# Kernel optimization log

Measured on AMD Instinct MI355X. Metric: run time of the kernel, lower is better.

The kernel has to match this reference:

```python
import jax, jax.numpy as jnp
import numpy as np

NUM_EMBEDDINGS = 512
EMBEDDING_DIM = 64
COMMITMENT_COST = 0.25
DECAY = 0.99
EPSILON = 1e-05


def setup_inputs() -> dict:
    key = jax.random.key(0)
    k1, k2, k3 = jax.random.split(key, 3)
    inputs = jax.random.normal(k1, (32, 64, 64, EMBEDDING_DIM), dtype=jnp.float32)
    emb_w = jax.random.normal(k2, (NUM_EMBEDDINGS, EMBEDDING_DIM), dtype=jnp.float32)
    ema_cluster_size = jnp.ones((NUM_EMBEDDINGS,), dtype=jnp.float32)
    ema_w = jax.random.normal(k3, (NUM_EMBEDDINGS, EMBEDDING_DIM), dtype=jnp.float32)
    return {"inputs": inputs, "emb_w": emb_w,
            "ema_cluster_size": ema_cluster_size, "ema_w": ema_w}


def reference(inputs, emb_w, ema_cluster_size, ema_w):
    """VQ-VAE EMA quantizer forward (training=True path).

    inputs:           [B, H, W, D]  NHWC latents
    emb_w:            [K, D]        codebook (pre-update)
    ema_cluster_size: [K]           EMA cluster-size buffer
    ema_w:            [K, D]        EMA weight buffer
    """
    B, H, W, D = inputs.shape
    K = emb_w.shape[0]
    flat = inputs.reshape(-1, D)                                  # [N, D]

    distances = (jnp.sum(flat * flat, axis=1, keepdims=True)
                 - 2.0 * flat @ emb_w.T
                 + jnp.sum(emb_w * emb_w, axis=1))
    encoding_indices = jnp.argmin(distances, axis=1)              # [N]
    encodings = jax.nn.one_hot(encoding_indices, K, dtype=flat.dtype)  # [N, K]

    # --- EMA codebook update (buffer math; no gradient flows here) ---
    counts = jax.lax.stop_gradient(jnp.sum(encodings, axis=0))    # [K]
    cs = ema_cluster_size * DECAY + (1.0 - DECAY) * counts
    n = jnp.sum(cs)
    cs = (cs + EPSILON) / (n + K * EPSILON) * n                   # Laplace smoothing
    dw = jax.ops.segment_sum(jax.lax.stop_gradient(flat),
                             encoding_indices, num_segments=K)    # [K, D]
    new_ema_w = ema_w * DECAY + (1.0 - DECAY) * dw
    new_emb = new_ema_w / cs[:, None]                             # updated codebook

    # Quantize with the updated codebook (gather)
    quantized = new_emb[encoding_indices].reshape(B, H, W, D)

    # Commitment loss (quantized is detached)
    e_latent_loss = jnp.mean((jax.lax.stop_gradient(quantized) - inputs) ** 2)
    loss = COMMITMENT_COST * e_latent_loss

    # Straight-through estimator
    quantized_st = inputs + jax.lax.stop_gradient(quantized - inputs)

    avg_probs = jnp.mean(encodings, axis=0)
    perplexity = jnp.exp(-jnp.sum(avg_probs * jnp.log(avg_probs + 1e-10)))

    # NHWC -> NCHW as in the original return
    return loss, jnp.transpose(quantized_st, (0, 3, 1, 2)), perplexity, encodings
```

## Files before the change

kernel.cpp:

```cpp
#include <hip/hip_runtime.h>

#define DIM 64
#define K_CODES 512
#define N_VEC 131072
#define NREP 16
#define Q_OFF 1
#define PERP_OFF 8388609
#define ENC_OFF 8388610

using bfrag = __attribute__((ext_vector_type(8))) short;
using ffrag = __attribute__((ext_vector_type(4))) float;

__device__ __forceinline__ void split3(float x, short& h0, short& h1, short& h2)
{
    unsigned u0 = __float_as_uint(x);
    h0 = (short)(u0 >> 16);
    float r = x - __uint_as_float(u0 & 0xFFFF0000u);
    unsigned u1 = __float_as_uint(r);
    h1 = (short)(u1 >> 16);
    float r2 = r - __uint_as_float(u1 & 0xFFFF0000u);
    h2 = (short)(__float_as_uint(r2) >> 16);
}

__global__ __launch_bounds__(256) void enc_zero_kernel(float* __restrict__ enc)
{
    const size_t nf4 = 16777215;
    float4* body = reinterpret_cast<float4*>(enc + 2);
    const size_t stride = (size_t)gridDim.x * 256;
    const float4 z = make_float4(0.f, 0.f, 0.f, 0.f);
    for (size_t i = (size_t)blockIdx.x * 256 + threadIdx.x; i < nf4; i += stride)
        body[i] = z;
    if (blockIdx.x == 0 && threadIdx.x == 0) {
        enc[0] = 0.f; enc[1] = 0.f;
        enc[67108862] = 0.f; enc[67108863] = 0.f;
    }
}

__global__ __launch_bounds__(64) void ee_kernel(const float* __restrict__ emb_w,
                                                float* __restrict__ ee)
{
    const int k = blockIdx.x * 64 + threadIdx.x;
    const float4* e4 = reinterpret_cast<const float4*>(emb_w + (size_t)k * DIM);
    float s0 = 0, s1 = 0, s2 = 0, s3 = 0;
#pragma unroll
    for (int d4 = 0; d4 < 16; ++d4) {
        const float4 v = e4[d4];
        s0 = fmaf(v.x, v.x, s0); s1 = fmaf(v.y, v.y, s1);
        s2 = fmaf(v.z, v.z, s2); s3 = fmaf(v.w, v.w, s3);
    }
    ee[k] = (s0 + s1) + (s2 + s3);
}

__global__ __launch_bounds__(256) void epack_kernel(const float* __restrict__ emb_w,
                                                    bfrag* __restrict__ epack)
{
    const int t = blockIdx.x * 256 + threadIdx.x;
    const int lane = t & 63;
    const int db = (t >> 6) & 1;
    const int ct = t >> 7;
    const int c  = ct * 16 + (lane & 15);
    const int d0 = db * 32 + (lane >> 4) * 8;
    const float* src = emb_w + (size_t)c * DIM + d0;
    bfrag f0, f1, f2;
#pragma unroll
    for (int j = 0; j < 8; ++j) {
        short a, b, cc;
        split3(src[j], a, b, cc);
        f0[j] = a; f1[j] = b; f2[j] = cc;
    }
    const int base = (ct * 2 + db) * 3;
    epack[(base + 0) * 64 + lane] = f0;
    epack[(base + 1) * 64 + lane] = f1;
    epack[(base + 2) * 64 + lane] = f2;
}

__global__ __launch_bounds__(256, 1) void argmin_mfma_kernel(
    const float* __restrict__ inputs,
    const bfrag* __restrict__ epack,
    const float* __restrict__ eeg,
    int* __restrict__ idx,
    float* __restrict__ counts_rep,
    float* __restrict__ enc)
{
    const int t = threadIdx.x;
    const int w = t >> 6;
    const int lane = t & 63;
    const int r16 = lane & 15;
    const int quad = lane >> 4;
    const size_t v0 = (size_t)blockIdx.x * 128 + w * 32;

    bfrag xf[2][2][3];
#pragma unroll
    for (int rt = 0; rt < 2; ++rt)
#pragma unroll
        for (int db = 0; db < 2; ++db) {
            const float* src = inputs + (v0 + rt * 16 + r16) * DIM + db * 32 + quad * 8;
            const float4 va = *reinterpret_cast<const float4*>(src);
            const float4 vb = *reinterpret_cast<const float4*>(src + 4);
            float vals[8] = {va.x, va.y, va.z, va.w, vb.x, vb.y, vb.z, vb.w};
            bfrag f0, f1, f2;
#pragma unroll
            for (int j = 0; j < 8; ++j) {
                short a, b, c;
                split3(vals[j], a, b, c);
                f0[j] = a; f1[j] = b; f2[j] = c;
            }
            xf[rt][db][0] = f0; xf[rt][db][1] = f1; xf[rt][db][2] = f2;
        }

    float best[2][4];
    int bestk[2][4];
#pragma unroll
    for (int a = 0; a < 2; ++a)
#pragma unroll
        for (int b = 0; b < 4; ++b) { best[a][b] = 3.4e38f; bestk[a][b] = 0; }

    constexpr int PI[6] = {0, 0, 1, 0, 2, 1};
    constexpr int PJ[6] = {0, 1, 0, 2, 0, 1};

    bfrag eC[2][3];
    float eelC;
#pragma unroll
    for (int db = 0; db < 2; ++db)
#pragma unroll
        for (int s = 0; s < 3; ++s)
            eC[db][s] = epack[(db * 3 + s) * 64 + lane];
    eelC = eeg[r16];

    for (int ct = 0; ct < 32; ++ct) {
        bfrag eN[2][3];
        float eelN = 0.f;
        if (ct < 31) {
#pragma unroll
            for (int db = 0; db < 2; ++db)
#pragma unroll
                for (int s = 0; s < 3; ++s)
                    eN[db][s] = epack[(((ct + 1) * 2 + db) * 3 + s) * 64 + lane];
            eelN = eeg[(ct + 1) * 16 + r16];
        }

        ffrag acc[2];
        acc[0] = (ffrag){0.f, 0.f, 0.f, 0.f};
        acc[1] = (ffrag){0.f, 0.f, 0.f, 0.f};
#pragma unroll
        for (int db = 0; db < 2; ++db)
#pragma unroll
            for (int p = 0; p < 6; ++p) {
                acc[0] = __builtin_amdgcn_mfma_f32_16x16x32_bf16(
                    xf[0][db][PI[p]], eC[db][PJ[p]], acc[0], 0, 0, 0);
                acc[1] = __builtin_amdgcn_mfma_f32_16x16x32_bf16(
                    xf[1][db][PI[p]], eC[db][PJ[p]], acc[1], 0, 0, 0);
            }

        const int kc = ct * 16 + r16;
#pragma unroll
        for (int rt = 0; rt < 2; ++rt)
#pragma unroll
            for (int rg = 0; rg < 4; ++rg) {
                const float dist = fmaf(-2.f, acc[rt][rg], eelC);
                if (dist < best[rt][rg]) { best[rt][rg] = dist; bestk[rt][rg] = kc; }
            }

#pragma unroll
        for (int db = 0; db < 2; ++db)
#pragma unroll
            for (int s = 0; s < 3; ++s)
                eC[db][s] = eN[db][s];
        eelC = eelN;
    }

#pragma unroll
    for (int rt = 0; rt < 2; ++rt)
#pragma unroll
        for (int rg = 0; rg < 4; ++rg) {
            float b = best[rt][rg];
            int k = bestk[rt][rg];
#pragma unroll
            for (int m = 1; m < 16; m <<= 1) {
                const float ob = __shfl_xor(b, m, 64);
                const int ok = __shfl_xor(k, m, 64);
                if (ob < b || (ob == b && ok < k)) { b = ob; k = ok; }
            }
            bestk[rt][rg] = k;
        }

    if (r16 == 0) {
        float* crep = counts_rep + (blockIdx.x & (NREP - 1)) * K_CODES;
#pragma unroll
        for (int rt = 0; rt < 2; ++rt)
#pragma unroll
            for (int rg = 0; rg < 4; ++rg) {
                const int v = rt * 16 + quad * 4 + rg;
                const int k = bestk[rt][rg];
                idx[v0 + v] = k;
                atomicAdd(&crep[k], 1.0f);
                enc[(v0 + v) * (size_t)K_CODES + k] = 1.0f;
            }
    }
}

__global__ __launch_bounds__(256) void dw_scatter_kernel(
    const float* __restrict__ inputs,
    const int* __restrict__ idx,
    float* __restrict__ dwrep)
{
    __shared__ int sIdx[256];
    const int t = threadIdx.x;
    const size_t vbase = (size_t)blockIdx.x * 256;
    sIdx[t] = idx[vbase + t];
    __syncthreads();
    const int w = t >> 6, lane = t & 63;
    const int v0 = w * 64;
#pragma unroll 4
    for (int j = 0; j < 64; ++j) {
        const int v = v0 + j;
        const int k = sIdx[v];
        const float xv = inputs[(vbase + v) * DIM + lane];
        atomicAdd(&dwrep[((v & (NREP - 1)) << 15) + (k << 6) + lane], xv);
    }
}

__global__ __launch_bounds__(512) void emaA_kernel(
    const float* __restrict__ counts_rep,
    const float* __restrict__ ema_cs,
    float* __restrict__ csbuf,
    float* __restrict__ perp_out)
{
    __shared__ float red[K_CODES];
    const int k = threadIdx.x;
    float cnt = 0.f;
#pragma unroll
    for (int r = 0; r < NREP; ++r) cnt += counts_rep[r * K_CODES + k];
    float cs = ema_cs[k] * 0.99f + 0.01f * cnt;

    red[k] = cs;
    __syncthreads();
    for (int s = K_CODES / 2; s > 0; s >>= 1) {
        if (k < s) red[k] += red[k + s];
        __syncthreads();
    }
    const float n = red[0];
    __syncthreads();

    csbuf[k] = (cs + 1e-5f) / (n + (float)K_CODES * 1e-5f) * n;

    const float p = cnt * (1.0f / (float)N_VEC);
    red[k] = p * logf(p + 1e-10f);
    __syncthreads();
    for (int s = K_CODES / 2; s > 0; s >>= 1) {
        if (k < s) red[k] += red[k + s];
        __syncthreads();
    }
    if (k == 0) perp_out[0] = expf(-red[0]);
}

__global__ __launch_bounds__(256) void emaB_kernel(
    const float* __restrict__ dwrep,
    const float* __restrict__ ema_w,
    const float* __restrict__ csbuf,
    float* __restrict__ new_emb)
{
    const int t = blockIdx.x * 256 + threadIdx.x;
    const int k = t >> 6;
    float dwv = 0.f;
#pragma unroll
    for (int r = 0; r < NREP; ++r) dwv += dwrep[(r << 15) + t];
    const float v = ema_w[t] * 0.99f + 0.01f * dwv;
    new_emb[t] = v / csbuf[k];
}

__global__ __launch_bounds__(256) void quantize_kernel(
    const float* __restrict__ inputs,
    const int* __restrict__ idx,
    const float* __restrict__ new_emb,
    float* __restrict__ out_q,
    float* __restrict__ loss_accum)
{
    __shared__ int sIdx[64];
    __shared__ float tile[DIM][65];
    __shared__ float wsum[4];

    const int bh = blockIdx.x;
    const int b = bh >> 6, h = bh & 63;
    const int t = threadIdx.x;

    if (t < 64) sIdx[t] = idx[bh * 64 + t];
    __syncthreads();

    const float* inRow = inputs + (size_t)bh * 64 * DIM;
    const int d = t & 63;
    const int wg = t >> 6;
    float lsum = 0.f;
#pragma unroll
    for (int p = 0; p < 16; ++p) {
        const int w = wg * 16 + p;
        const float xv = inRow[w * DIM + d];
        const float qv = new_emb[sIdx[w] * DIM + d];
        const float diff = qv - xv;
        tile[d][w] = xv + diff;
        lsum = fmaf(diff, diff, lsum);
    }
    __syncthreads();

    const int w2 = t & 63;
    const int dg = t >> 6;
#pragma unroll
    for (int p = 0; p < 16; ++p) {
        const int d2 = dg * 16 + p;
        out_q[(((size_t)b * DIM + d2) * 64 + h) * 64 + w2] = tile[d2][w2];
    }

    for (int off = 32; off > 0; off >>= 1) lsum += __shfl_down(lsum, off);
    if ((t & 63) == 0) wsum[t >> 6] = lsum;
    __syncthreads();
    if (t == 0) atomicAdd(loss_accum, (wsum[0] + wsum[1]) + (wsum[2] + wsum[3]));
}

__global__ void finalize_kernel(const float* __restrict__ loss_accum,
                                float* __restrict__ out_loss)
{
    out_loss[0] = 0.25f * (loss_accum[0] / 8388608.0f);
}

extern "C" void kernel_launch(void* const* d_in, const int* in_sizes, int n_in,
                              void* d_out, int out_size, void* d_ws, size_t ws_size,
                              hipStream_t stream)
{
    const float* inputs = (const float*)d_in[0];
    const float* emb_w  = (const float*)d_in[1];
    const float* ema_cs = (const float*)d_in[2];
    const float* ema_w  = (const float*)d_in[3];
    float* out = (float*)d_out;
    float* ws  = (float*)d_ws;

    int*   idxbuf  = (int*)ws;
    float* crep    = ws + 131072;
    float* lossac  = ws + 139264;
    float* csbuf   = ws + 139265;
    float* eebuf   = ws + 139777;
    float* nemb    = ws + 140289;
    bfrag* epack   = (bfrag*)(ws + 173060);

    float* dwrep = out + 16;

    hipMemsetAsync(crep, 0, (NREP * K_CODES + 1) * sizeof(float), stream);
    hipMemsetAsync(dwrep, 0, NREP * K_CODES * DIM * sizeof(float), stream);

    ee_kernel<<<K_CODES / 64, 64, 0, stream>>>(emb_w, eebuf);
    epack_kernel<<<16, 256, 0, stream>>>(emb_w, epack);

    enc_zero_kernel<<<2048, 256, 0, stream>>>(out + ENC_OFF);

    argmin_mfma_kernel<<<N_VEC / 128, 256, 0, stream>>>(
        inputs, epack, eebuf, idxbuf, crep, out + ENC_OFF);

    dw_scatter_kernel<<<N_VEC / 256, 256, 0, stream>>>(inputs, idxbuf, dwrep);

    emaA_kernel<<<1, K_CODES, 0, stream>>>(crep, ema_cs, csbuf, out + PERP_OFF);
    emaB_kernel<<<K_CODES * DIM / 256, 256, 0, stream>>>(dwrep, ema_w, csbuf, nemb);

    quantize_kernel<<<32 * 64, 256, 0, stream>>>(
        inputs, idxbuf, nemb, out + Q_OFF, lossac);

    finalize_kernel<<<1, 1, 0, stream>>>(lossac, out);
}
```

Before: 226.0 us.

## Fuse one-hot write and dw scatter into argmin kernel, halve rows per wave

Drops the separate zero-fill kernel for the encodings matrix. The argmin kernel now writes each full one-hot row with float2 stores. The dw segment-sum scatter is also folded into the argmin kernel, rebuilding x from its three bf16 splits already held in registers instead of re-reading inputs. Each wave now handles 16 rows instead of 32, with two blocks per CU. This removes a 256MB zero pass and a kernel launch, but halves MFMA reuse of each codebook fragment and relies on the bf16 split sum reproducing x exactly.

```diff
diff --git a/kernel.cpp b/kernel.cpp
--- a/kernel.cpp
+++ b/kernel.cpp
@@ -22,24 +22,15 @@
     h2 = (short)(__float_as_uint(r2) >> 16);
 }
 
-__global__ __launch_bounds__(256) void enc_zero_kernel(float* __restrict__ enc)
-{
-    const size_t nf4 = 16777215;
-    float4* body = reinterpret_cast<float4*>(enc + 2);
-    const size_t stride = (size_t)gridDim.x * 256;
-    const float4 z = make_float4(0.f, 0.f, 0.f, 0.f);
-    for (size_t i = (size_t)blockIdx.x * 256 + threadIdx.x; i < nf4; i += stride)
-        body[i] = z;
-    if (blockIdx.x == 0 && threadIdx.x == 0) {
-        enc[0] = 0.f; enc[1] = 0.f;
-        enc[67108862] = 0.f; enc[67108863] = 0.f;
-    }
-}
-
-__global__ __launch_bounds__(64) void ee_kernel(const float* __restrict__ emb_w,
-                                                float* __restrict__ ee)
-{
-    const int k = blockIdx.x * 64 + threadIdx.x;
+__device__ __forceinline__ float b2f(short h)
+{
+    return __uint_as_float(((unsigned)(unsigned short)h) << 16);
+}
+
+__global__ __launch_bounds__(512) void ee_kernel(const float* __restrict__ emb_w,
+                                                 float* __restrict__ ee)
+{
+    const int k = threadIdx.x;
     const float4* e4 = reinterpret_cast<const float4*>(emb_w + (size_t)k * DIM);
     float s0 = 0, s1 = 0, s2 = 0, s3 = 0;
 #pragma unroll
@@ -74,46 +65,44 @@
     epack[(base + 2) * 64 + lane] = f2;
 }
 
-__global__ __launch_bounds__(256, 1) void argmin_mfma_kernel(
+__global__ __launch_bounds__(256, 2) void argmin_mfma_kernel(
     const float* __restrict__ inputs,
     const bfrag* __restrict__ epack,
     const float* __restrict__ eeg,
     int* __restrict__ idx,
     float* __restrict__ counts_rep,
+    float* __restrict__ dwrep,
     float* __restrict__ enc)
 {
+    __shared__ int sBK[64];
+
     const int t = threadIdx.x;
-    const int w = t >> 6;
+    const int wv = t >> 6;
     const int lane = t & 63;
     const int r16 = lane & 15;
     const int quad = lane >> 4;
-    const size_t v0 = (size_t)blockIdx.x * 128 + w * 32;
-
-    bfrag xf[2][2][3];
-#pragma unroll
-    for (int rt = 0; rt < 2; ++rt)
-#pragma unroll
-        for (int db = 0; db < 2; ++db) {
-            const float* src = inputs + (v0 + rt * 16 + r16) * DIM + db * 32 + quad * 8;
-            const float4 va = *reinterpret_cast<const float4*>(src);
-            const float4 vb = *reinterpret_cast<const float4*>(src + 4);
-            float vals[8] = {va.x, va.y, va.z, va.w, vb.x, vb.y, vb.z, vb.w};
-            bfrag f0, f1, f2;
-#pragma unroll
-            for (int j = 0; j < 8; ++j) {
-                short a, b, c;
-                split3(vals[j], a, b, c);
-                f0[j] = a; f1[j] = b; f2[j] = c;
-            }
-            xf[rt][db][0] = f0; xf[rt][db][1] = f1; xf[rt][db][2] = f2;
-        }
-
-    float best[2][4];
-    int bestk[2][4];
-#pragma unroll
-    for (int a = 0; a < 2; ++a)
-#pragma unroll
-        for (int b = 0; b < 4; ++b) { best[a][b] = 3.4e38f; bestk[a][b] = 0; }
+    const size_t v0 = (size_t)blockIdx.x * 64 + wv * 16;
+    const int rep = blockIdx.x & (NREP - 1);
+
+    bfrag xf[2][3];
+#pragma unroll
+    for (int db = 0; db < 2; ++db) {
+        const float* src = inputs + (v0 + r16) * DIM + db * 32 + quad * 8;
+        const float4 va = *reinterpret_cast<const float4*>(src);
+        const float4 vb = *reinterpret_cast<const float4*>(src + 4);
+        float vals[8] = {va.x, va.y, va.z, va.w, vb.x, vb.y, vb.z, vb.w};
+        bfrag f0, f1, f2;
+#pragma unroll
+        for (int j = 0; j < 8; ++j) {
+            short a, b, c;
+            split3(vals[j], a, b, c);
+            f0[j] = a; f1[j] = b; f2[j] = c;
+        }
+        xf[db][0] = f0; xf[db][1] = f1; xf[db][2] = f2;
+    }
+
+    float best[4] = {3.4e38f, 3.4e38f, 3.4e38f, 3.4e38f};
+    int bestk[4] = {0, 0, 0, 0};
 
     constexpr int PI[6] = {0, 0, 1, 0, 2, 1};
     constexpr int PJ[6] = {0, 1, 0, 2, 0, 1};
@@ -139,27 +128,20 @@
             eelN = eeg[(ct + 1) * 16 + r16];
         }
 
-        ffrag acc[2];
-        acc[0] = (ffrag){0.f, 0.f, 0.f, 0.f};
-        acc[1] = (ffrag){0.f, 0.f, 0.f, 0.f};
+        ffrag acc = (ffrag){0.f, 0.f, 0.f, 0.f};
 #pragma unroll
         for (int db = 0; db < 2; ++db)
 #pragma unroll
-            for (int p = 0; p < 6; ++p) {
-                acc[0] = __builtin_amdgcn_mfma_f32_16x16x32_bf16(
-                    xf[0][db][PI[p]], eC[db][PJ[p]], acc[0], 0, 0, 0);
-                acc[1] = __builtin_amdgcn_mfma_f32_16x16x32_bf16(
-                    xf[1][db][PI[p]], eC[db][PJ[p]], acc[1], 0, 0, 0);
-            }
+            for (int p = 0; p < 6; ++p)
+                acc = __builtin_amdgcn_mfma_f32_16x16x32_bf16(
+                    xf[db][PI[p]], eC[db][PJ[p]], acc, 0, 0, 0);
 
         const int kc = ct * 16 + r16;
 #pragma unroll
-        for (int rt = 0; rt < 2; ++rt)
-#pragma unroll
-            for (int rg = 0; rg < 4; ++rg) {
-                const float dist = fmaf(-2.f, acc[rt][rg], eelC);
-                if (dist < best[rt][rg]) { best[rt][rg] = dist; bestk[rt][rg] = kc; }
-            }
+        for (int rg = 0; rg < 4; ++rg) {
+            const float dist = fmaf(-2.f, acc[rg], eelC);
+            if (dist < best[rg]) { best[rg] = dist; bestk[rg] = kc; }
+        }
 
 #pragma unroll
         for (int db = 0; db < 2; ++db)
@@ -170,53 +152,56 @@
     }
 
 #pragma unroll
-    for (int rt = 0; rt < 2; ++rt)
+    for (int rg = 0; rg < 4; ++rg) {
+        float b = best[rg];
+        int k = bestk[rg];
+#pragma unroll
+        for (int m = 1; m < 16; m <<= 1) {
+            const float ob = __shfl_xor(b, m, 64);
+            const int ok = __shfl_xor(k, m, 64);
+            if (ob < b || (ob == b && ok < k)) { b = ob; k = ok; }
+        }
+        bestk[rg] = k;
+    }
+
+    if (r16 == 0) {
+        float* crep = counts_rep + rep * K_CODES;
 #pragma unroll
         for (int rg = 0; rg < 4; ++rg) {
-            float b = best[rt][rg];
-            int k = bestk[rt][rg];
-#pragma unroll
-            for (int m = 1; m < 16; m <<= 1) {
-                const float ob = __shfl_xor(b, m, 64);
-                const int ok = __shfl_xor(k, m, 64);
-                if (ob < b || (ob == b && ok < k)) { b = ob; k = ok; }
+            const int v = quad * 4 + rg;
+            const int k = bestk[rg];
+            sBK[wv * 16 + v] = k;
+            idx[v0 + v] = k;
+            atomicAdd(&crep[k], 1.0f);
+        }
+    }
+
+#pragma unroll 4
+    for (int v = 0; v < 16; ++v) {
+        const int bk = sBK[wv * 16 + v];
+        float* rowp = enc + (v0 + v) * (size_t)K_CODES;
+#pragma unroll
+        for (int part = 0; part < 4; ++part) {
+            const int c0 = part * 128 + lane * 2;
+            float2 val;
+            val.x = (c0 == bk) ? 1.0f : 0.0f;
+            val.y = (c0 + 1 == bk) ? 1.0f : 0.0f;
+            *reinterpret_cast<float2*>(rowp + c0) = val;
+        }
+    }
+
+    {
+        const int myk = sBK[wv * 16 + r16];
+        float* dwr = dwrep + ((size_t)rep * K_CODES + myk) * DIM;
+#pragma unroll
+        for (int db = 0; db < 2; ++db)
+#pragma unroll
+            for (int j = 0; j < 8; ++j) {
+                const int d = db * 32 + quad * 8 + j;
+                const float val =
+                    (b2f(xf[db][0][j]) + b2f(xf[db][1][j])) + b2f(xf[db][2][j]);
+                atomicAdd(&dwr[d], val);
             }
-            bestk[rt][rg] = k;
-        }
-
-    if (r16 == 0) {
-        float* crep = counts_rep + (blockIdx.x & (NREP - 1)) * K_CODES;
-#pragma unroll
-        for (int rt = 0; rt < 2; ++rt)
-#pragma unroll
-            for (int rg = 0; rg < 4; ++rg) {
-                const int v = rt * 16 + quad * 4 + rg;
-                const int k = bestk[rt][rg];
-                idx[v0 + v] = k;
-                atomicAdd(&crep[k], 1.0f);
-                enc[(v0 + v) * (size_t)K_CODES + k] = 1.0f;
-            }
-    }
-}
-
-__global__ __launch_bounds__(256) void dw_scatter_kernel(
-    const float* __restrict__ inputs,
-    const int* __restrict__ idx,
-    float* __restrict__ dwrep)
-{
-    __shared__ int sIdx[256];
-    const int t = threadIdx.x;
-    const size_t vbase = (size_t)blockIdx.x * 256;
-    sIdx[t] = idx[vbase + t];
-    __syncthreads();
-    const int w = t >> 6, lane = t & 63;
-    const int v0 = w * 64;
-#pragma unroll 4
-    for (int j = 0; j < 64; ++j) {
-        const int v = v0 + j;
-        const int k = sIdx[v];
-        const float xv = inputs[(vbase + v) * DIM + lane];
-        atomicAdd(&dwrep[((v & (NREP - 1)) << 15) + (k << 6) + lane], xv);
     }
 }
 
@@ -346,15 +331,11 @@
     hipMemsetAsync(crep, 0, (NREP * K_CODES + 1) * sizeof(float), stream);
     hipMemsetAsync(dwrep, 0, NREP * K_CODES * DIM * sizeof(float), stream);
 
-    ee_kernel<<<K_CODES / 64, 64, 0, stream>>>(emb_w, eebuf);
+    ee_kernel<<<1, K_CODES, 0, stream>>>(emb_w, eebuf);
     epack_kernel<<<16, 256, 0, stream>>>(emb_w, epack);
 
-    enc_zero_kernel<<<2048, 256, 0, stream>>>(out + ENC_OFF);
-
-    argmin_mfma_kernel<<<N_VEC / 128, 256, 0, stream>>>(
-        inputs, epack, eebuf, idxbuf, crep, out + ENC_OFF);
-
-    dw_scatter_kernel<<<N_VEC / 256, 256, 0, stream>>>(inputs, idxbuf, dwrep);
+    argmin_mfma_kernel<<<N_VEC / 64, 256, 0, stream>>>(
+        inputs, epack, eebuf, idxbuf, crep, dwrep, out + ENC_OFF);
 
     emaA_kernel<<<1, K_CODES, 0, stream>>>(crep, ema_cs, csbuf, out + PERP_OFF);
     emaB_kernel<<<K_CODES * DIM / 256, 256, 0, stream>>>(dwrep, ema_w, csbuf, nemb);
```

Measured after the change: 458.8 us. 103% more time.
